# Kernel tuning notes

Measured on AMD Instinct MI355X. Metric: run time of the kernel, lower is better.

The kernel has to match this reference:

```python
import jax, jax.numpy as jnp
import numpy as np

N_NODES = 4096
IN_FEAT = 256
N_HEADS = 8
N_HIDDEN = 32  # out_features // n_heads
NEG_SLOPE = 0.2


def setup_inputs() -> dict:
    key = jax.random.key(0)
    k1, k2, k3, k4 = jax.random.split(key, 4)
    h = jax.random.normal(k1, (N_NODES, IN_FEAT), dtype=jnp.float32)
    W = jax.random.normal(k2, (N_HEADS * N_HIDDEN, IN_FEAT), dtype=jnp.float32) * 0.05
    a = jax.random.normal(k3, (2 * N_HIDDEN,), dtype=jnp.float32) * 0.05
    adj_mat = jax.random.randint(k4, (N_NODES, N_NODES, 1), 0, 2, dtype=jnp.int32)
    return {"h": h, "W": W, "a": a, "adj_mat": adj_mat}


def reference(h, W, a, adj_mat):
    n = h.shape[0]
    # g = linear(h) -> [N, H, F]
    g = (h @ W.T).reshape(n, N_HEADS, N_HIDDEN)
    # e_ij = LeakyReLU(a^T [g_i || g_j]) = LeakyReLU(a_l . g_i + a_r . g_j)
    a_l, a_r = a[:N_HIDDEN], a[N_HIDDEN:]
    s_i = jnp.einsum('nhf,f->nh', g, a_l)  # destination term (repeat_interleave axis)
    s_j = jnp.einsum('nhf,f->nh', g, a_r)  # source term (repeat axis)
    e = jax.nn.leaky_relu(s_i[:, None, :] + s_j[None, :, :], NEG_SLOPE)  # [N, N, H]
    e = jnp.where(adj_mat == 0, jnp.float32(-jnp.inf), e)
    att = jax.nn.softmax(e, axis=1)  # softmax over source nodes j
    # dropout(p) in eval mode -> identity
    out = jnp.einsum('ijh,jhf->ihf', att, g)
    return out.reshape(n, N_HEADS * N_HIDDEN)  # is_concat=True
```

## Files before the change

### kernel.cpp

```cpp
#include <hip/hip_runtime.h>
#include <hip/hip_bf16.h>
#include <math.h>

constexpr int N   = 4096;
constexpr int F   = 256;
constexpr int NH  = 8;
constexpr int HID = 32;
constexpr float SLOPE = 0.2f;

using frag_ab  = __attribute__((ext_vector_type(8))) short;
using frag_cd  = __attribute__((ext_vector_type(4))) float;
using frag_c16 = __attribute__((ext_vector_type(16))) float;

__device__ inline unsigned short f2bf(float x) {
  unsigned int u = __float_as_uint(x);
  unsigned int r = (u + 0x7fffu + ((u >> 16) & 1u)) >> 16;
  return (unsigned short)r;
}

__global__ __launch_bounds__(256) void k_pre(const float* __restrict__ h,
                                             const float* __restrict__ W,
                                             const float* __restrict__ a,
                                             const int* __restrict__ adj,
                                             unsigned short* __restrict__ hb,
                                             float* __restrict__ U,
                                             unsigned int* __restrict__ bits,
                                             float* __restrict__ outp,
                                             float* __restrict__ lbuf) {
  const int b = blockIdx.x, t = threadIdx.x;
  if (b < 544) {
    const int idx8 = (b * 256 + t) * 8;
    const float* src = (idx8 < N * F) ? (h + idx8) : (W + idx8 - N * F);
    const float4 v0 = *(const float4*)src;
    const float4 v1 = *(const float4*)(src + 4);
    unsigned short tmp[8];
    tmp[0] = f2bf(v0.x); tmp[1] = f2bf(v0.y); tmp[2] = f2bf(v0.z); tmp[3] = f2bf(v0.w);
    tmp[4] = f2bf(v1.x); tmp[5] = f2bf(v1.y); tmp[6] = f2bf(v1.z); tmp[7] = f2bf(v1.w);
    *(int4*)(hb + idx8) = *(int4*)tmp;
  } else if (b < 560) {
    const int c = b - 544, k = t;
    const int head = c & 7, side = c >> 3;
    float acc = 0.f;
#pragma unroll
    for (int f = 0; f < 32; ++f)
      acc += W[(size_t)(head * 32 + f) * F + k] * a[side * 32 + f];
    U[c * F + k] = acc;
  } else if (b < 2608) {
    const int lane = t & 63, w = t >> 6;
    const int row  = (b - 560) * 2 + (w >> 1);
    const int half = w & 1;
    const int4* arow = (const int4*)(adj + (size_t)row * N) + half * 512;
    unsigned int* brow = bits + (size_t)row * (N / 32) + half * 64;
#pragma unroll
    for (int c = 0; c < 8; ++c) {
      const int4 av = arow[c * 64 + lane];
      unsigned int v = (av.x != 0 ? 1u : 0u) | (av.y != 0 ? 2u : 0u) |
                       (av.z != 0 ? 4u : 0u) | (av.w != 0 ? 8u : 0u);
      v <<= ((lane & 7) * 4);
      v |= __shfl_xor(v, 1);
      v |= __shfl_xor(v, 2);
      v |= __shfl_xor(v, 4);
      if ((lane & 7) == 0) brow[c * 8 + (lane >> 3)] = v;
    }
  } else if (b < 2864) {
    const int base = (b - 2608) * 256 + t;
#pragma unroll
    for (int q = 0; q < 4; ++q)
      *(float4*)(outp + ((size_t)q * 65536 + base) * 4) =
          make_float4(0.f, 0.f, 0.f, 0.f);
  } else {
    *(float4*)(lbuf + ((size_t)(b - 2864) * 256 + t) * 4) =
        make_float4(0.f, 0.f, 0.f, 0.f);
  }
}

__global__ __launch_bounds__(256) void k_mid(const float* __restrict__ h,
                                             const float* __restrict__ U,
                                             const unsigned short* __restrict__ hb,
                                             const unsigned short* __restrict__ Wb,
                                             float* __restrict__ RT,
                                             unsigned int* __restrict__ BDT,
                                             unsigned short* __restrict__ gT) {
  __shared__ float hs[16][260];
  __shared__ float Us[16][260];
  const int b = blockIdx.x, t = threadIdx.x;
  if (b < 256) {
    const int i0 = b * 16;
    {
      const int r = t >> 4, s0 = (t & 15) * 16;
      const float4* src = (const float4*)(h + (size_t)(i0 + r) * F + s0);
      const float4* usr = (const float4*)(U + (size_t)r * F + s0);
#pragma unroll
      for (int q = 0; q < 4; ++q) {
        *(float4*)&hs[r][s0 + q * 4] = src[q];
        *(float4*)&Us[r][s0 + q * 4] = usr[q];
      }
    }
    __syncthreads();
    const int r = t >> 4, c = t & 15;
    float acc = 0.f;
#pragma unroll
    for (int k4 = 0; k4 < 64; ++k4) {
      const float4 hv = *(const float4*)&hs[r][k4 * 4];
      const float4 uv = *(const float4*)&Us[c][k4 * 4];
      acc += hv.x * uv.x + hv.y * uv.y + hv.z * uv.z + hv.w * uv.w;
    }
    const int n = i0 + r;
    if (c < 8) {
      RT[(size_t)n * NH + c] = __expf(-0.8f * acc);
    } else {
      const int hd = c - 8;
      const unsigned int bw = f2bf(__expf(acc));
      const unsigned int dw = f2bf(__expf(SLOPE * acc));
      BDT[(size_t)hd * N + n] = (bw << 16) | dw;
    }
  } else {
    const int lane = t & 63;
    const int tile = (b - 256) * 4 + (t >> 6);
    const int mt = tile >> 4, nt = tile & 15;
    const int m0 = mt * 16, n0 = nt * 16;
    const int n16 = lane & 15, quad = lane >> 4;
    frag_cd acc = {0.f, 0.f, 0.f, 0.f};
    const unsigned short* ap = hb + (size_t)(m0 + n16) * F + quad * 8;
    const unsigned short* bp = Wb + (size_t)(n0 + n16) * F + quad * 8;
#pragma unroll
    for (int ks = 0; ks < F / 32; ++ks) {
      const frag_ab af = *(const frag_ab*)(ap + ks * 32);
      const frag_ab bf = *(const frag_ab*)(bp + ks * 32);
      acc = __builtin_amdgcn_mfma_f32_16x16x32_bf16(af, bf, acc, 0, 0, 0);
    }
    unsigned short tmp[4];
#pragma unroll
    for (int reg = 0; reg < 4; ++reg) tmp[reg] = f2bf(acc[reg]);
    *(int2*)(gT + (size_t)(n0 + n16) * N + m0 + quad * 4) = *(int2*)tmp;
  }
}

constexpr int TI = 32;
constexpr int NSPLIT = 4;

__global__ __launch_bounds__(256, 6) void k_agg(
    const unsigned short* __restrict__ gT,
    const float* __restrict__ RT,
    const unsigned int* __restrict__ BDT,
    const unsigned int* __restrict__ bits,
    float* __restrict__ outp, float* __restrict__ lbuf) {
  __shared__ __align__(16) unsigned short sB[64][140];
  __shared__ __align__(16) unsigned int sBD[2][128];

  const int t    = threadIdx.x;
  const int lane = t & 63;
  const int wv   = t >> 6;
  const int hd   = wv >> 1;
  const int jh   = wv & 1;
  const int b    = blockIdx.x;
  const int hp   = b & 3;
  const int js   = (b >> 2) & (NSPLIT - 1);
  const int i0   = (b >> 4) * TI;
  const int head = hp * 2 + hd;

  const int n32 = lane & 31;
  const int kh  = lane >> 5;

  const int myi  = i0 + n32;
  const float Ri = RT[(size_t)myi * NH + head];
  const uint4* bp4 = (const uint4*)(bits + (size_t)myi * (N / 32) + js * 32);

  frag_c16 acc = {0.f, 0.f, 0.f, 0.f, 0.f, 0.f, 0.f, 0.f,
                  0.f, 0.f, 0.f, 0.f, 0.f, 0.f, 0.f, 0.f};
  float lpart = 0.f;

  const int sr = t >> 2, ss0 = t & 3;
  const unsigned short* gsrc = gT + (size_t)(hp * 64 + sr) * N + js * 1024;
  const unsigned int*  bdsrc = BDT + (size_t)(hp * 2 + (t >> 7)) * N + js * 1024 + (t & 127);

  for (int c8 = 0; c8 < 8; ++c8) {
    __syncthreads();
    {
#pragma unroll
      for (int s = 0; s < 4; ++s) {
        const int seg = ss0 + s * 4;
        const int4 v = *(const int4*)(gsrc + c8 * 128 + seg * 8);
        *(int2*)&sB[sr][seg * 8]     = make_int2(v.x, v.y);
        *(int2*)&sB[sr][seg * 8 + 4] = make_int2(v.z, v.w);
      }
    }
    sBD[t >> 7][t & 127] = bdsrc[c8 * 128];
    const uint4 bw = bp4[c8];
    __syncthreads();
#pragma unroll
    for (int sh = 0; sh < 4; ++sh) {
      const int ss = sh * 2 + jh;
      const int jb = ss * 16 + kh * 8;
      const uint4 bdl = *(const uint4*)&sBD[hd][jb];
      const uint4 bdh = *(const uint4*)&sBD[hd][jb + 4];
      const unsigned int w32 =
          (ss >> 1) == 0 ? bw.x : (ss >> 1) == 1 ? bw.y : (ss >> 1) == 2 ? bw.z : bw.w;
      const unsigned int mb = (w32 >> (((ss & 1) << 4) + (kh << 3))) & 0xFFu;

      const unsigned int bdw[8] = {bdl.x, bdl.y, bdl.z, bdl.w,
                                   bdh.x, bdh.y, bdh.z, bdh.w};
      int packed[4];
#pragma unroll
      for (int p = 0; p < 4; ++p) {
        const unsigned int u0 = bdw[2 * p], u1 = bdw[2 * p + 1];
        const float B0 = __uint_as_float(u0 & 0xFFFF0000u);
        const float D0 = __uint_as_float(u0 << 16);
        const float B1 = __uint_as_float(u1 & 0xFFFF0000u);
        const float D1 = __uint_as_float(u1 << 16);
        float w0 = fmaxf(B0, Ri * D0);
        float w1 = fmaxf(B1, Ri * D1);
        w0 = (mb & (1u << (2 * p)))     ? w0 : 0.f;
        w1 = (mb & (1u << (2 * p + 1))) ? w1 : 0.f;
        lpart += w0 + w1;
        const __hip_bfloat162 bp2 = __float22bfloat162_rn(make_float2(w0, w1));
        __builtin_memcpy(&packed[p], &bp2, 4);
      }
      frag_ab af;
      __builtin_memcpy(&af, packed, 16);

      const int frow = hd * 32 + n32;
      const int2 blo = *(const int2*)&sB[frow][jb];
      const int2 bhi = *(const int2*)&sB[frow][jb + 4];
      const int bt[4] = {blo.x, blo.y, bhi.x, bhi.y};
      frag_ab bf;
      __builtin_memcpy(&bf, bt, 16);

      acc = __builtin_amdgcn_mfma_f32_32x32x16_bf16(af, bf, acc, 0, 0, 0);
    }
  }

  float* mrg  = (float*)&sB[0][0];
  float* mrgl = (float*)&sBD[0][0];
  const float lp2 = lpart + __shfl_xor(lpart, 32);
  __syncthreads();
  if (jh == 1) {
#pragma unroll
    for (int reg = 0; reg < 16; ++reg) {
      const int row = (reg & 3) + 8 * (reg >> 2) + 4 * kh;
      mrg[(size_t)(hd * 32 + row) * 32 + n32] = acc[reg];
    }
    if (kh == 0) mrgl[hd * 32 + n32] = lp2;
  }
  __syncthreads();
  if (jh == 0) {
    const float lt = lp2 + mrgl[hd * 32 + n32];
    if (kh == 0) atomicAdd(&lbuf[(size_t)(i0 + n32) * NH + head], lt);
#pragma unroll
    for (int reg = 0; reg < 16; ++reg) {
      const int row = (reg & 3) + 8 * (reg >> 2) + 4 * kh;
      const float v = acc[reg] + mrg[(size_t)(hd * 32 + row) * 32 + n32];
      atomicAdd(&outp[(size_t)(i0 + row) * F + head * HID + n32], v);
    }
  }
}

__global__ __launch_bounds__(256) void k_norm(float* __restrict__ outp,
                                              const float* __restrict__ lbuf) {
  const int idx = blockIdx.x * 256 + threadIdx.x;
  const int i = idx >> 6, fq = idx & 63;
  const int hh = fq >> 3;
  const float inv = 1.f / lbuf[(size_t)i * NH + hh];
  float4 v = *(float4*)(outp + (size_t)idx * 4);
  v.x *= inv; v.y *= inv; v.z *= inv; v.w *= inv;
  *(float4*)(outp + (size_t)idx * 4) = v;
}

extern "C" void kernel_launch(void* const* d_in, const int* in_sizes, int n_in,
                              void* d_out, int out_size, void* d_ws, size_t ws_size,
                              hipStream_t stream) {
  const float* h   = (const float*)d_in[0];
  const float* W   = (const float*)d_in[1];
  const float* a   = (const float*)d_in[2];
  const int*   adj = (const int*)d_in[3];
  float* out = (float*)d_out;

  char* ws = (char*)d_ws;
  unsigned short* hb = (unsigned short*)ws;  ws += (size_t)(N * F + F * F) * 2;
  unsigned short* Wb = hb + (size_t)N * F;
  unsigned short* gT = (unsigned short*)ws;  ws += (size_t)N * F * 2;
  unsigned int* bits = (unsigned int*)ws;    ws += (size_t)N * (N / 32) * 4;
  float* U    = (float*)ws;                  ws += 16 * F * 4;
  float* RT   = (float*)ws;                  ws += (size_t)N * NH * 4;
  unsigned int* BDT = (unsigned int*)ws;     ws += (size_t)N * NH * 4;
  float* lbuf = (float*)ws;                  ws += (size_t)N * NH * 4;

  k_pre<<<dim3(2896), dim3(256), 0, stream>>>(h, W, a, adj, hb, U, bits, out, lbuf);
  k_mid<<<dim3(1280), dim3(256), 0, stream>>>(h, U, hb, Wb, RT, BDT, gT);
  k_agg<<<dim3((N / TI) * 4 * NSPLIT), dim3(256), 0, stream>>>(
      gT, RT, BDT, bits, out, lbuf);
  k_norm<<<dim3(N * F / 4 / 256), dim3(256), 0, stream>>>(out, lbuf);
}
```

Baseline: 164.0 us.

## Switch attention weights and features to fp16 with packed half2 weight math

Converts the bf16 pipeline to fp16. The projection GEMM and aggregation MFMAs now use f16 instructions, and attention weights are computed as packed half2 max/multiply with bitmask-based zeroing. The row sum uses fdot2 instead of per-element float conversion and bf16 repacking. The B/D exponent tables are now separate fp16 arrays read directly from global memory into registers rather than staged through shared memory. This is meant to cut ALU work in the inner aggregation loop, but exp values risk fp16 overflow or underflow beyond about 65504.

```diff
diff --git a/kernel.cpp b/kernel.cpp
--- a/kernel.cpp
+++ b/kernel.cpp
@@ -1,5 +1,4 @@
 #include <hip/hip_runtime.h>
-#include <hip/hip_bf16.h>
 #include <math.h>
 
 constexpr int N   = 4096;
@@ -8,14 +7,14 @@
 constexpr int HID = 32;
 constexpr float SLOPE = 0.2f;
 
-using frag_ab  = __attribute__((ext_vector_type(8))) short;
+using h2       = __attribute__((ext_vector_type(2))) _Float16;
+using frag_f16 = __attribute__((ext_vector_type(8))) _Float16;
 using frag_cd  = __attribute__((ext_vector_type(4))) float;
 using frag_c16 = __attribute__((ext_vector_type(16))) float;
 
-__device__ inline unsigned short f2bf(float x) {
-  unsigned int u = __float_as_uint(x);
-  unsigned int r = (u + 0x7fffu + ((u >> 16) & 1u)) >> 16;
-  return (unsigned short)r;
+__device__ inline unsigned short f2h(float x) {
+  _Float16 v = (_Float16)x;
+  unsigned short u; __builtin_memcpy(&u, &v, 2); return u;
 }
 
 __global__ __launch_bounds__(256) void k_pre(const float* __restrict__ h,
@@ -34,8 +33,8 @@
     const float4 v0 = *(const float4*)src;
     const float4 v1 = *(const float4*)(src + 4);
     unsigned short tmp[8];
-    tmp[0] = f2bf(v0.x); tmp[1] = f2bf(v0.y); tmp[2] = f2bf(v0.z); tmp[3] = f2bf(v0.w);
-    tmp[4] = f2bf(v1.x); tmp[5] = f2bf(v1.y); tmp[6] = f2bf(v1.z); tmp[7] = f2bf(v1.w);
+    tmp[0] = f2h(v0.x); tmp[1] = f2h(v0.y); tmp[2] = f2h(v0.z); tmp[3] = f2h(v0.w);
+    tmp[4] = f2h(v1.x); tmp[5] = f2h(v1.y); tmp[6] = f2h(v1.z); tmp[7] = f2h(v1.w);
     *(int4*)(hb + idx8) = *(int4*)tmp;
   } else if (b < 560) {
     const int c = b - 544, k = t;
@@ -78,8 +77,9 @@
                                              const float* __restrict__ U,
                                              const unsigned short* __restrict__ hb,
                                              const unsigned short* __restrict__ Wb,
-                                             float* __restrict__ RT,
-                                             unsigned int* __restrict__ BDT,
+                                             unsigned int* __restrict__ RT2,
+                                             unsigned short* __restrict__ BT,
+                                             unsigned short* __restrict__ DT,
                                              unsigned short* __restrict__ gT) {
   __shared__ float hs[16][260];
   __shared__ float Us[16][260];
@@ -107,12 +107,12 @@
     }
     const int n = i0 + r;
     if (c < 8) {
-      RT[(size_t)n * NH + c] = __expf(-0.8f * acc);
+      const unsigned int r16 = f2h(__expf(-0.8f * acc));
+      RT2[(size_t)n * NH + c] = (r16 << 16) | r16;
     } else {
       const int hd = c - 8;
-      const unsigned int bw = f2bf(__expf(acc));
-      const unsigned int dw = f2bf(__expf(SLOPE * acc));
-      BDT[(size_t)hd * N + n] = (bw << 16) | dw;
+      BT[(size_t)hd * N + n] = f2h(__expf(acc));
+      DT[(size_t)hd * N + n] = f2h(__expf(SLOPE * acc));
     }
   } else {
     const int lane = t & 63;
@@ -125,13 +125,13 @@
     const unsigned short* bp = Wb + (size_t)(n0 + n16) * F + quad * 8;
 #pragma unroll
     for (int ks = 0; ks < F / 32; ++ks) {
-      const frag_ab af = *(const frag_ab*)(ap + ks * 32);
-      const frag_ab bf = *(const frag_ab*)(bp + ks * 32);
-      acc = __builtin_amdgcn_mfma_f32_16x16x32_bf16(af, bf, acc, 0, 0, 0);
+      const frag_f16 af = *(const frag_f16*)(ap + ks * 32);
+      const frag_f16 bf = *(const frag_f16*)(bp + ks * 32);
+      acc = __builtin_amdgcn_mfma_f32_16x16x32_f16(af, bf, acc, 0, 0, 0);
     }
     unsigned short tmp[4];
 #pragma unroll
-    for (int reg = 0; reg < 4; ++reg) tmp[reg] = f2bf(acc[reg]);
+    for (int reg = 0; reg < 4; ++reg) tmp[reg] = f2h(acc[reg]);
     *(int2*)(gT + (size_t)(n0 + n16) * N + m0 + quad * 4) = *(int2*)tmp;
   }
 }
@@ -141,12 +141,12 @@
 
 __global__ __launch_bounds__(256, 6) void k_agg(
     const unsigned short* __restrict__ gT,
-    const float* __restrict__ RT,
-    const unsigned int* __restrict__ BDT,
+    const unsigned int* __restrict__ RT2,
+    const unsigned short* __restrict__ BT, const unsigned short* __restrict__ DT,
     const unsigned int* __restrict__ bits,
     float* __restrict__ outp, float* __restrict__ lbuf) {
   __shared__ __align__(16) unsigned short sB[64][140];
-  __shared__ __align__(16) unsigned int sBD[2][128];
+  __shared__ float sMl[2][32];
 
   const int t    = threadIdx.x;
   const int lane = t & 63;
@@ -161,18 +161,25 @@
 
   const int n32 = lane & 31;
   const int kh  = lane >> 5;
-
-  const int myi  = i0 + n32;
-  const float Ri = RT[(size_t)myi * NH + head];
+  const int shmb = jh * 16 + kh * 8;
+
+  const int myi = i0 + n32;
+  const unsigned int Ri2u = RT2[(size_t)myi * NH + head];
+  h2 Ri2; __builtin_memcpy(&Ri2, &Ri2u, 4);
   const uint4* bp4 = (const uint4*)(bits + (size_t)myi * (N / 32) + js * 32);
+
+  const unsigned short* BTh = BT + (size_t)head * N + js * 1024;
+  const unsigned short* DTh = DT + (size_t)head * N + js * 1024;
 
   frag_c16 acc = {0.f, 0.f, 0.f, 0.f, 0.f, 0.f, 0.f, 0.f,
                   0.f, 0.f, 0.f, 0.f, 0.f, 0.f, 0.f, 0.f};
   float lpart = 0.f;
+#if __has_builtin(__builtin_amdgcn_fdot2)
+  const h2 one2 = {(_Float16)1.0f, (_Float16)1.0f};
+#endif
 
   const int sr = t >> 2, ss0 = t & 3;
   const unsigned short* gsrc = gT + (size_t)(hp * 64 + sr) * N + js * 1024;
-  const unsigned int*  bdsrc = BDT + (size_t)(hp * 2 + (t >> 7)) * N + js * 1024 + (t & 127);
 
   for (int c8 = 0; c8 < 8; ++c8) {
     __syncthreads();
@@ -185,53 +192,54 @@
         *(int2*)&sB[sr][seg * 8 + 4] = make_int2(v.z, v.w);
       }
     }
-    sBD[t >> 7][t & 127] = bdsrc[c8 * 128];
+    uint4 Bv[4], Dv[4];
+#pragma unroll
+    for (int sh = 0; sh < 4; ++sh) {
+      const int jb = (sh * 2 + jh) * 16 + kh * 8;
+      Bv[sh] = *(const uint4*)(BTh + c8 * 128 + jb);
+      Dv[sh] = *(const uint4*)(DTh + c8 * 128 + jb);
+    }
     const uint4 bw = bp4[c8];
+    const unsigned int bwa[4] = {bw.x, bw.y, bw.z, bw.w};
     __syncthreads();
 #pragma unroll
     for (int sh = 0; sh < 4; ++sh) {
-      const int ss = sh * 2 + jh;
-      const int jb = ss * 16 + kh * 8;
-      const uint4 bdl = *(const uint4*)&sBD[hd][jb];
-      const uint4 bdh = *(const uint4*)&sBD[hd][jb + 4];
-      const unsigned int w32 =
-          (ss >> 1) == 0 ? bw.x : (ss >> 1) == 1 ? bw.y : (ss >> 1) == 2 ? bw.z : bw.w;
-      const unsigned int mb = (w32 >> (((ss & 1) << 4) + (kh << 3))) & 0xFFu;
-
-      const unsigned int bdw[8] = {bdl.x, bdl.y, bdl.z, bdl.w,
-                                   bdh.x, bdh.y, bdh.z, bdh.w};
-      int packed[4];
+      const int jb = (sh * 2 + jh) * 16 + kh * 8;
+      const unsigned int mb = (bwa[sh] >> shmb) & 0xFFu;
+      const unsigned int bu[4] = {Bv[sh].x, Bv[sh].y, Bv[sh].z, Bv[sh].w};
+      const unsigned int du[4] = {Dv[sh].x, Dv[sh].y, Dv[sh].z, Dv[sh].w};
+      unsigned int packed[4];
 #pragma unroll
       for (int p = 0; p < 4; ++p) {
-        const unsigned int u0 = bdw[2 * p], u1 = bdw[2 * p + 1];
-        const float B0 = __uint_as_float(u0 & 0xFFFF0000u);
-        const float D0 = __uint_as_float(u0 << 16);
-        const float B1 = __uint_as_float(u1 & 0xFFFF0000u);
-        const float D1 = __uint_as_float(u1 << 16);
-        float w0 = fmaxf(B0, Ri * D0);
-        float w1 = fmaxf(B1, Ri * D1);
-        w0 = (mb & (1u << (2 * p)))     ? w0 : 0.f;
-        w1 = (mb & (1u << (2 * p + 1))) ? w1 : 0.f;
-        lpart += w0 + w1;
-        const __hip_bfloat162 bp2 = __float22bfloat162_rn(make_float2(w0, w1));
-        __builtin_memcpy(&packed[p], &bp2, 4);
+        h2 hB, hD;
+        __builtin_memcpy(&hB, &bu[p], 4);
+        __builtin_memcpy(&hD, &du[p], 4);
+        const h2 wm = __builtin_elementwise_max(hB, Ri2 * hD);
+        unsigned int wp; __builtin_memcpy(&wp, &wm, 4);
+        const unsigned int d  = (mb >> (2 * p)) & 3u;
+        const unsigned int sp = ((d | (d << 15)) & 0x10001u) * 0xFFFFu;
+        wp &= sp;
+        packed[p] = wp;
+        h2 wh; __builtin_memcpy(&wh, &wp, 4);
+#if __has_builtin(__builtin_amdgcn_fdot2)
+        lpart = __builtin_amdgcn_fdot2(wh, one2, lpart, false);
+#else
+        lpart += (float)wh.x + (float)wh.y;
+#endif
       }
-      frag_ab af;
-      __builtin_memcpy(&af, packed, 16);
+      frag_f16 af; __builtin_memcpy(&af, packed, 16);
 
       const int frow = hd * 32 + n32;
       const int2 blo = *(const int2*)&sB[frow][jb];
       const int2 bhi = *(const int2*)&sB[frow][jb + 4];
       const int bt[4] = {blo.x, blo.y, bhi.x, bhi.y};
-      frag_ab bf;
-      __builtin_memcpy(&bf, bt, 16);
-
-      acc = __builtin_amdgcn_mfma_f32_32x32x16_bf16(af, bf, acc, 0, 0, 0);
-    }
-  }
-
-  float* mrg  = (float*)&sB[0][0];
-  float* mrgl = (float*)&sBD[0][0];
+      frag_f16 bf; __builtin_memcpy(&bf, bt, 16);
+
+      acc = __builtin_amdgcn_mfma_f32_32x32x16_f16(af, bf, acc, 0, 0, 0);
+    }
+  }
+
+  float* mrg = (float*)&sB[0][0];
   const float lp2 = lpart + __shfl_xor(lpart, 32);
   __syncthreads();
   if (jh == 1) {
@@ -240,11 +248,11 @@
       const int row = (reg & 3) + 8 * (reg >> 2) + 4 * kh;
       mrg[(size_t)(hd * 32 + row) * 32 + n32] = acc[reg];
     }
-    if (kh == 0) mrgl[hd * 32 + n32] = lp2;
+    if (kh == 0) sMl[hd][n32] = lp2;
   }
   __syncthreads();
   if (jh == 0) {
-    const float lt = lp2 + mrgl[hd * 32 + n32];
+    const float lt = lp2 + sMl[hd][n32];
     if (kh == 0) atomicAdd(&lbuf[(size_t)(i0 + n32) * NH + head], lt);
 #pragma unroll
     for (int reg = 0; reg < 16; ++reg) {
@@ -281,13 +289,14 @@
   unsigned short* gT = (unsigned short*)ws;  ws += (size_t)N * F * 2;
   unsigned int* bits = (unsigned int*)ws;    ws += (size_t)N * (N / 32) * 4;
   float* U    = (float*)ws;                  ws += 16 * F * 4;
-  float* RT   = (float*)ws;                  ws += (size_t)N * NH * 4;
-  unsigned int* BDT = (unsigned int*)ws;     ws += (size_t)N * NH * 4;
+  unsigned int* RT2 = (unsigned int*)ws;     ws += (size_t)N * NH * 4;
+  unsigned short* BT = (unsigned short*)ws;  ws += (size_t)N * NH * 2;
+  unsigned short* DT = (unsigned short*)ws;  ws += (size_t)N * NH * 2;
   float* lbuf = (float*)ws;                  ws += (size_t)N * NH * 4;
 
   k_pre<<<dim3(2896), dim3(256), 0, stream>>>(h, W, a, adj, hb, U, bits, out, lbuf);
-  k_mid<<<dim3(1280), dim3(256), 0, stream>>>(h, U, hb, Wb, RT, BDT, gT);
+  k_mid<<<dim3(1280), dim3(256), 0, stream>>>(h, U, hb, Wb, RT2, BT, DT, gT);
   k_agg<<<dim3((N / TI) * 4 * NSPLIT), dim3(256), 0, stream>>>(
-      gT, RT, BDT, bits, out, lbuf);
+      gT, RT2, BT, DT, bits, out, lbuf);
   k_norm<<<dim3(N * F / 4 / 256), dim3(256), 0, stream>>>(out, lbuf);
 }
```

Measured after the change: 157.5 us. 1.04x faster.
